# Performance work log

Hardware: AMD Instinct MI355X
Metric: run time of the kernel (lower is better)

## Reference

```python
import jax, jax.numpy as jnp
import numpy as np

COMMITMENT_COST = 0.25


def setup_inputs() -> dict:
    key = jax.random.key(0)
    k1, k2 = jax.random.split(key, 2)
    inputs = jax.random.normal(k1, (8, 2048, 1024), dtype=jnp.float32)
    # per-head codebooks: [H=4, K=1024, dh=256]
    codebook = jax.random.normal(k2, (4, 1024, 256), dtype=jnp.float32)
    return {"inputs": inputs, "codebook": codebook}


def reference(inputs, codebook):
    H, K, dh = codebook.shape
    flat = inputs.reshape(-1, H, dh)  # [N, H, dh]
    # squared-euclidean distances per head: [H, N, K]
    x_sq = jnp.sum(flat * flat, axis=-1).T[:, :, None]          # [H, N, 1]
    c_sq = jnp.sum(codebook * codebook, axis=-1)[:, None, :]    # [H, 1, K]
    dots = jnp.einsum('nhd,hkd->hnk', flat, codebook)           # [H, N, K]
    distances = x_sq + c_sq - 2.0 * dots
    idx = jnp.argmin(distances, axis=-1)                        # [H, N]
    # gather codebook rows (equivalent to one-hot @ codebook)
    q = jnp.take_along_axis(codebook, idx[:, :, None], axis=1)  # [H, N, dh]
    quantized = jnp.transpose(q, (1, 0, 2)).reshape(inputs.shape)
    # ema=True, eval mode: q_latent_loss = 0
    e_latent_loss = jnp.mean((jax.lax.stop_gradient(quantized) - inputs) ** 2)
    loss = COMMITMENT_COST * e_latent_loss
    # residual=False: straight-through estimator
    quantized_out = inputs + jax.lax.stop_gradient(quantized - inputs)
    return loss, quantized_out
```

## Files before the change

kernel.cpp:

```cpp
#include <hip/hip_runtime.h>
#include <cfloat>

#define NH    4
#define NK    1024
#define DHD   256
#define NTOK  16384
#define ROWS  (NH * DHD)

typedef __attribute__((ext_vector_type(8))) short bf16x8;
typedef __attribute__((ext_vector_type(4))) float f32x4;

#define WS_CSQ  ((size_t)0)
#define WS_BH   ((size_t)16384)
#define WS_BL   (WS_BH + (size_t)2097152)
#define WS_NEED (WS_BL + (size_t)2097152)

__device__ __forceinline__ unsigned short f32_to_bf16_rn(float f) {
    unsigned u = __float_as_uint(f);
    u += 0x7FFFu + ((u >> 16) & 1u);
    return (unsigned short)(u >> 16);
}
__device__ __forceinline__ float bf16_as_f32(unsigned short h) {
    return __uint_as_float(((unsigned)h) << 16);
}

__device__ __forceinline__ void gload_lds16(const uint4* g, uint4* l) {
    __builtin_amdgcn_global_load_lds(
        (const __attribute__((address_space(1))) void*)g,
        (__attribute__((address_space(3))) void*)l, 16, 0, 0);
}

__global__ __launch_bounds__(64) void csq_kernel(const float* __restrict__ cb,
                                                 float* __restrict__ csq) {
    const int code = blockIdx.x;
    const int lane = threadIdx.x;
    const float4 v = *(const float4*)(cb + (size_t)code * DHD + lane * 4);
    float s = v.x * v.x + v.y * v.y + v.z * v.z + v.w * v.w;
#pragma unroll
    for (int off = 32; off > 0; off >>= 1) s += __shfl_down(s, off, 64);
    if (lane == 0) csq[code] = s;
}

__global__ __launch_bounds__(256) void cvt_cb_kernel(const float* __restrict__ cb,
                                                     uint4* __restrict__ bch,
                                                     uint4* __restrict__ bcl) {
    const int g = blockIdx.x * 8 + (threadIdx.x >> 5);
    const int o = threadIdx.x & 31;
    const float* src = cb + (size_t)g * DHD + o * 8;
    unsigned wh[4], wl[4];
#pragma unroll
    for (int i = 0; i < 4; ++i) {
        const float f0 = src[2 * i], f1 = src[2 * i + 1];
        const unsigned short h0 = f32_to_bf16_rn(f0);
        const unsigned short h1 = f32_to_bf16_rn(f1);
        const unsigned short l0 = f32_to_bf16_rn(f0 - bf16_as_f32(h0));
        const unsigned short l1 = f32_to_bf16_rn(f1 - bf16_as_f32(h1));
        wh[i] = (unsigned)h0 | ((unsigned)h1 << 16);
        wl[i] = (unsigned)l0 | ((unsigned)l1 << 16);
    }
    const int hh = g >> 10, c = g & 1023, dc = o >> 2, kk = o & 3;
    const size_t unit = (size_t)((hh * 8 + dc) * 4 + kk) * NK + c;
    bch[unit] = make_uint4(wh[0], wh[1], wh[2], wh[3]);
    bcl[unit] = make_uint4(wl[0], wl[1], wl[2], wl[3]);
}

__device__ __forceinline__ bool lt_vi(float v, int i, float w, int j) {
    return (v < w) || (v == w && i < j);
}

__device__ __forceinline__ float np_sq_pairwise256(const float* __restrict__ a) {
#pragma clang fp contract(off)
    float tot = 0.f;
#pragma unroll
    for (int blk = 0; blk < 2; ++blk) {
        const float* p = a + blk * 128;
        float r0 = p[0] * p[0], r1 = p[1] * p[1], r2 = p[2] * p[2], r3 = p[3] * p[3];
        float r4 = p[4] * p[4], r5 = p[5] * p[5], r6 = p[6] * p[6], r7 = p[7] * p[7];
#pragma clang loop unroll_count(2)
        for (int i = 8; i < 128; i += 8) {
            r0 = r0 + p[i + 0] * p[i + 0];
            r1 = r1 + p[i + 1] * p[i + 1];
            r2 = r2 + p[i + 2] * p[i + 2];
            r3 = r3 + p[i + 3] * p[i + 3];
            r4 = r4 + p[i + 4] * p[i + 4];
            r5 = r5 + p[i + 5] * p[i + 5];
            r6 = r6 + p[i + 6] * p[i + 6];
            r7 = r7 + p[i + 7] * p[i + 7];
        }
        const float res = ((r0 + r1) + (r2 + r3)) + ((r4 + r5) + (r6 + r7));
        tot = (blk == 0) ? res : (tot + res);
    }
    return tot;
}

__device__ __forceinline__ float np_dot_seq256(const float* __restrict__ a,
                                               const float* __restrict__ b) {
#pragma clang fp contract(off)
    float s = 0.f;
#pragma clang loop unroll_count(4)
    for (int i = 0; i < 256; ++i) s = s + a[i] * b[i];
    return s;
}

__global__ __launch_bounds__(256, 2) void vq_mfma(const float* __restrict__ x,
                                                  const float* __restrict__ cb,
                                                  const float* __restrict__ csq,
                                                  const uint4* __restrict__ bch,
                                                  const uint4* __restrict__ bcl,
                                                  float* __restrict__ out) {
    __shared__ uint4 BsH[2048];
    __shared__ uint4 BsL[2048];
    __shared__ float Cs[NK];
    __shared__ int   Cand[128][2];
    __shared__ int   SIdx[128];
    __shared__ float WSum[4];

    const int tid  = threadIdx.x;
    const int h    = blockIdx.y;
    const int t0   = blockIdx.x * 128;
    const int wv   = tid >> 6;
    const int lane = tid & 63;
    const int kk   = lane >> 4;
    const int ln   = lane & 15;

    const float* xh  = x  + (size_t)t0 * ROWS + h * DHD;
    const float* cbh = cb + (size_t)h * NK * DHD;

#pragma unroll
    for (int i = tid; i < NK; i += 256) Cs[i] = csq[h * NK + i];

    bf16x8 aH[2][8], aL[2][8];
    {
        const int tokb = t0 + wv * 32 + ln;
        const float* xa = x + (size_t)tokb * ROWS + h * DHD + kk * 8;
#pragma unroll
        for (int rt = 0; rt < 2; ++rt) {
#pragma unroll
            for (int dc = 0; dc < 8; ++dc) {
                const float* p = xa + (size_t)(rt * 16) * ROWS + dc * 32;
                const float4 f0 = *(const float4*)p;
                const float4 f1 = *(const float4*)(p + 4);
                const float f[8] = {f0.x, f0.y, f0.z, f0.w, f1.x, f1.y, f1.z, f1.w};
                bf16x8 hv, lv;
#pragma unroll
                for (int j = 0; j < 8; ++j) {
                    const unsigned short hb = f32_to_bf16_rn(f[j]);
                    hv[j] = (short)hb;
                    lv[j] = (short)f32_to_bf16_rn(f[j] - bf16_as_f32(hb));
                }
                aH[rt][dc] = hv;
                aL[rt][dc] = lv;
            }
        }
    }

    float b1[8], b2[8];
    int   i1[8], i2[8];
#pragma unroll
    for (int s = 0; s < 8; ++s) { b1[s] = FLT_MAX; b2[s] = FLT_MAX; i1[s] = 0; i2[s] = 0; }

    for (int k0 = 0; k0 < NK; k0 += 64) {
        __syncthreads();
#pragma unroll
        for (int p = 0; p < 8; ++p) {
            const size_t w = (size_t)(h * 32 + p * 4 + wv) * NK + k0 + lane;
            gload_lds16(&bch[w], &BsH[p * 256 + wv * 64]);
            gload_lds16(&bcl[w], &BsL[p * 256 + wv * 64]);
        }
        __syncthreads();

        f32x4 acc[2][4];
#pragma unroll
        for (int rt = 0; rt < 2; ++rt)
#pragma unroll
            for (int ct = 0; ct < 4; ++ct) acc[rt][ct] = (f32x4){0.f, 0.f, 0.f, 0.f};

#pragma unroll
        for (int dc = 0; dc < 8; ++dc) {
#pragma unroll
            for (int ct = 0; ct < 4; ++ct) {
                const int bu = (dc * 4 + kk) * 64 + ct * 16 + ln;
                const bf16x8 bH = *(const bf16x8*)&BsH[bu];
                const bf16x8 bL = *(const bf16x8*)&BsL[bu];
#pragma unroll
                for (int rt = 0; rt < 2; ++rt) {
                    acc[rt][ct] = __builtin_amdgcn_mfma_f32_16x16x32_bf16(aH[rt][dc], bH, acc[rt][ct], 0, 0, 0);
                    acc[rt][ct] = __builtin_amdgcn_mfma_f32_16x16x32_bf16(aH[rt][dc], bL, acc[rt][ct], 0, 0, 0);
                    acc[rt][ct] = __builtin_amdgcn_mfma_f32_16x16x32_bf16(aL[rt][dc], bH, acc[rt][ct], 0, 0, 0);
                }
            }
        }

#pragma unroll
        for (int rt = 0; rt < 2; ++rt)
#pragma unroll
            for (int ct = 0; ct < 4; ++ct) {
                const float cs   = Cs[k0 + ct * 16 + ln];
                const int   codg = k0 + ct * 16 + ln;
#pragma unroll
                for (int r = 0; r < 4; ++r) {
                    const float dist = cs - 2.f * acc[rt][ct][r];
                    const int   s    = rt * 4 + r;
                    if (dist < b1[s]) { b2[s] = b1[s]; i2[s] = i1[s]; b1[s] = dist; i1[s] = codg; }
                    else if (dist < b2[s]) { b2[s] = dist; i2[s] = codg; }
                }
            }
    }

#pragma unroll
    for (int s = 0; s < 8; ++s) {
        float v1 = b1[s], v2 = b2[s];
        int   j1 = i1[s], j2 = i2[s];
#pragma unroll
        for (int m = 1; m <= 8; m <<= 1) {
            const float o1 = __shfl_xor(v1, m, 64);
            const int   oj1 = __shfl_xor(j1, m, 64);
            const float o2 = __shfl_xor(v2, m, 64);
            const int   oj2 = __shfl_xor(j2, m, 64);
            if (lt_vi(o1, oj1, v1, j1)) {
                if (lt_vi(v1, j1, o2, oj2)) { v2 = v1; j2 = j1; }
                else                        { v2 = o2; j2 = oj2; }
                v1 = o1; j1 = oj1;
            } else if (lt_vi(o1, oj1, v2, j2)) {
                v2 = o1; j2 = oj1;
            }
        }
        if (ln == 0) {
            const int tl = wv * 32 + (s >> 2) * 16 + kk * 4 + (s & 3);
            Cand[tl][0] = j1;
            Cand[tl][1] = j2;
        }
    }
    __syncthreads();

    {
        const int token = tid >> 1;
        const int cand  = tid & 1;
        const int code  = Cand[token][cand];
        const float* xr = xh + (size_t)token * ROWS;
        const float* cr = cbh + (size_t)code * DHD;
        const float X = np_sq_pairwise256(xr);
        const float C = np_sq_pairwise256(cr);
        const float D = np_dot_seq256(xr, cr);
        float d;
        {
#pragma clang fp contract(off)
            const float t = X + C;
            d = t - 2.0f * D;
        }
        const float od = __shfl_xor(d, 1, 64);
        if (cand == 0) {
            const int jA = code;
            const int jB = Cand[token][1];
            const bool pickB = (od < d) || (od == d && jB < jA);
            SIdx[token] = pickB ? jB : jA;
        }
    }
    __syncthreads();

    float lacc = 0.f;
    for (int t = wv; t < 128; t += 4) {
        const float4 q4 = *(const float4*)(cbh + (size_t)SIdx[t] * DHD + (lane << 2));
        const float4 x4 = *(const float4*)(xh + (size_t)t * ROWS + (lane << 2));
        const float dx = q4.x - x4.x, dy = q4.y - x4.y;
        const float dz = q4.z - x4.z, dw = q4.w - x4.w;
        lacc += dx * dx + dy * dy + dz * dz + dw * dw;
        *(float4*)(out + 1 + (size_t)(t0 + t) * ROWS + h * DHD + (lane << 2)) = q4;
    }
#pragma unroll
    for (int off = 32; off > 0; off >>= 1) lacc += __shfl_down(lacc, off, 64);
    if (lane == 0) WSum[wv] = lacc;
    __syncthreads();
    if (tid == 0) {
        const float s = WSum[0] + WSum[1] + WSum[2] + WSum[3];
        atomicAdd(out, s * (0.25f / 16777216.f));
    }
}

#define TN 128
#define TK 128
#define KC 16
#define APAD 4
#define BPAD 4

__global__ __launch_bounds__(256, 2) void vq_main_fp32(const float* __restrict__ x,
                                                       const float* __restrict__ cb,
                                                       const float* __restrict__ csq,
                                                       float* __restrict__ out) {
    __shared__ float As[KC][TN + APAD];
    __shared__ float Bs[KC][TK + BPAD];
    __shared__ float Cs[TK];
    __shared__ int   Cand[TN][2];
    __shared__ int   SIdx[TN];
    __shared__ float WSum[4];

    const int tid = threadIdx.x;
    const int h   = blockIdx.y;
    const int t0  = blockIdx.x * TN;
    const int ty  = tid >> 4;
    const int tx  = tid & 15;

    const float* xh  = x  + (size_t)t0 * ROWS + h * DHD;
    const float* cbh = cb + (size_t)h * NK * DHD;

    const int sr = tid >> 1;
    const int sd = (tid & 1) << 3;

    float b1[8], b2[8];
    int   i1[8], i2[8];
#pragma unroll
    for (int r = 0; r < 8; ++r) { b1[r] = FLT_MAX; b2[r] = FLT_MAX; i1[r] = 0; i2[r] = 0; }

    for (int k0 = 0; k0 < NK; k0 += TK) {
        __syncthreads();
        if (tid < TK) Cs[tid] = csq[h * NK + k0 + tid];

        float acc[8][8];
#pragma unroll
        for (int r = 0; r < 8; ++r)
#pragma unroll
            for (int c = 0; c < 8; ++c) acc[r][c] = 0.f;

        for (int d0 = 0; d0 < DHD; d0 += KC) {
            __syncthreads();
            {
                const float* ap = xh + (size_t)sr * ROWS + d0 + sd;
                const float4 a0 = *(const float4*)ap;
                const float4 a1 = *(const float4*)(ap + 4);
                As[sd + 0][sr] = a0.x; As[sd + 1][sr] = a0.y;
                As[sd + 2][sr] = a0.z; As[sd + 3][sr] = a0.w;
                As[sd + 4][sr] = a1.x; As[sd + 5][sr] = a1.y;
                As[sd + 6][sr] = a1.z; As[sd + 7][sr] = a1.w;
            }
            {
                const float* bp = cbh + (size_t)(k0 + sr) * DHD + d0 + sd;
                const float4 b0v = *(const float4*)bp;
                const float4 b1v = *(const float4*)(bp + 4);
                Bs[sd + 0][sr] = b0v.x; Bs[sd + 1][sr] = b0v.y;
                Bs[sd + 2][sr] = b0v.z; Bs[sd + 3][sr] = b0v.w;
                Bs[sd + 4][sr] = b1v.x; Bs[sd + 5][sr] = b1v.y;
                Bs[sd + 6][sr] = b1v.z; Bs[sd + 7][sr] = b1v.w;
            }
            __syncthreads();
#pragma unroll 4
            for (int kc = 0; kc < KC; ++kc) {
                const float4 a0 = *(const float4*)&As[kc][ty << 3];
                const float4 a1 = *(const float4*)&As[kc][(ty << 3) + 4];
                const float4 p0 = *(const float4*)&Bs[kc][tx << 2];
                const float4 p1 = *(const float4*)&Bs[kc][64 + (tx << 2)];
                const float aa[8] = {a0.x, a0.y, a0.z, a0.w, a1.x, a1.y, a1.z, a1.w};
                const float bb[8] = {p0.x, p0.y, p0.z, p0.w, p1.x, p1.y, p1.z, p1.w};
#pragma unroll
                for (int r = 0; r < 8; ++r)
#pragma unroll
                    for (int c = 0; c < 8; ++c)
                        acc[r][c] = fmaf(aa[r], bb[c], acc[r][c]);
            }
        }
#pragma unroll
        for (int r = 0; r < 8; ++r) {
#pragma unroll
            for (int c = 0; c < 8; ++c) {
                const int cc = (c < 4) ? ((tx << 2) + c) : (64 + (tx << 2) + c - 4);
                const float dist = Cs[cc] - 2.f * acc[r][c];
                const int   idx  = k0 + cc;
                if (dist < b1[r]) { b2[r] = b1[r]; i2[r] = i1[r]; b1[r] = dist; i1[r] = idx; }
                else if (dist < b2[r]) { b2[r] = dist; i2[r] = idx; }
            }
        }
    }

#pragma unroll
    for (int r = 0; r < 8; ++r) {
        float v1 = b1[r], v2 = b2[r];
        int   j1 = i1[r], j2 = i2[r];
#pragma unroll
        for (int m = 1; m <= 8; m <<= 1) {
            const float o1 = __shfl_xor(v1, m, 64);
            const int   oj1 = __shfl_xor(j1, m, 64);
            const float o2 = __shfl_xor(v2, m, 64);
            const int   oj2 = __shfl_xor(j2, m, 64);
            if (lt_vi(o1, oj1, v1, j1)) {
                if (lt_vi(v1, j1, o2, oj2)) { v2 = v1; j2 = j1; }
                else                        { v2 = o2; j2 = oj2; }
                v1 = o1; j1 = oj1;
            } else if (lt_vi(o1, oj1, v2, j2)) {
                v2 = o1; j2 = oj1;
            }
        }
        b1[r] = v1; i1[r] = j1; b2[r] = v2; i2[r] = j2;
    }
    if (tx == 0) {
#pragma unroll
        for (int r = 0; r < 8; ++r) {
            Cand[(ty << 3) + r][0] = i1[r];
            Cand[(ty << 3) + r][1] = i2[r];
        }
    }
    __syncthreads();

    {
        const int token = tid >> 1;
        const int cand  = tid & 1;
        const int code  = Cand[token][cand];
        const float* xr = xh + (size_t)token * ROWS;
        const float* cr = cbh + (size_t)code * DHD;
        const float X = np_sq_pairwise256(xr);
        const float C = np_sq_pairwise256(cr);
        const float D = np_dot_seq256(xr, cr);
        float d;
        {
#pragma clang fp contract(off)
            const float t = X + C;
            d = t - 2.0f * D;
        }
        const float od = __shfl_xor(d, 1, 64);
        if (cand == 0) {
            const int jA = code;
            const int jB = Cand[token][1];
            const bool pickB = (od < d) || (od == d && jB < jA);
            SIdx[token] = pickB ? jB : jA;
        }
    }
    __syncthreads();

    const int wav  = tid >> 6;
    const int lane = tid & 63;
    float lacc = 0.f;
    for (int t = wav; t < TN; t += 4) {
        const float4 q4 = *(const float4*)(cbh + (size_t)SIdx[t] * DHD + (lane << 2));
        const float4 x4 = *(const float4*)(xh + (size_t)t * ROWS + (lane << 2));
        const float dx = q4.x - x4.x, dy = q4.y - x4.y;
        const float dz = q4.z - x4.z, dw = q4.w - x4.w;
        lacc += dx * dx + dy * dy + dz * dz + dw * dw;
        *(float4*)(out + 1 + (size_t)(t0 + t) * ROWS + h * DHD + (lane << 2)) = q4;
    }
#pragma unroll
    for (int off = 32; off > 0; off >>= 1) lacc += __shfl_down(lacc, off, 64);
    if (lane == 0) WSum[wav] = lacc;
    __syncthreads();
    if (tid == 0) {
        const float s = WSum[0] + WSum[1] + WSum[2] + WSum[3];
        atomicAdd(out, s * (0.25f / 16777216.f));
    }
}

extern "C" void kernel_launch(void* const* d_in, const int* in_sizes, int n_in,
                              void* d_out, int out_size, void* d_ws, size_t ws_size,
                              hipStream_t stream) {
    const float* x   = (const float*)d_in[0];
    const float* cb  = (const float*)d_in[1];
    float*       out = (float*)d_out;
    char*        ws  = (char*)d_ws;
    float*       csq = (float*)(ws + WS_CSQ);

    hipMemsetAsync(d_out, 0, sizeof(float), stream);
    csq_kernel<<<NH * NK, 64, 0, stream>>>(cb, csq);

    if (ws_size >= WS_NEED) {
        uint4* bch = (uint4*)(ws + WS_BH);
        uint4* bcl = (uint4*)(ws + WS_BL);
        cvt_cb_kernel<<<NH * NK / 8, 256, 0, stream>>>(cb, bch, bcl);
        dim3 grid(NTOK / 128, NH);
        vq_mfma<<<grid, 256, 0, stream>>>(x, cb, csq, bch, bcl, out);
    } else {
        dim3 grid(NTOK / TN, NH);
        vq_main_fp32<<<grid, 256, 0, stream>>>(x, cb, csq, out);
    }
}
```

Before: 329.4 us.

## Double-buffer codebook tiles, swizzle block order, and fuse exact refinement loads

Measured after the change: 378.4 us. 14.9% more time.

```diff
diff --git a/kernel.cpp b/kernel.cpp
--- a/kernel.cpp
+++ b/kernel.cpp
@@ -102,22 +102,91 @@
     return s;
 }
 
+__device__ __forceinline__ void refine_exact(const float* __restrict__ xr,
+                                             const float* __restrict__ cr,
+                                             float& Xo, float& Co, float& Do) {
+#pragma clang fp contract(off)
+    const float4* xq = (const float4*)xr;
+    const float4* cq = (const float4*)cr;
+    float xa[8], ca[8];
+    float xres0 = 0.f, cres0 = 0.f;
+    float s = 0.f;
+#pragma unroll
+    for (int c = 0; c < 8; ++c) {
+        float xf[32], cf[32];
+#pragma unroll
+        for (int q = 0; q < 8; ++q) {
+            const float4 a = xq[c * 8 + q];
+            const float4 b = cq[c * 8 + q];
+            xf[q * 4 + 0] = a.x; xf[q * 4 + 1] = a.y;
+            xf[q * 4 + 2] = a.z; xf[q * 4 + 3] = a.w;
+            cf[q * 4 + 0] = b.x; cf[q * 4 + 1] = b.y;
+            cf[q * 4 + 2] = b.z; cf[q * 4 + 3] = b.w;
+        }
+        if (c == 0 || c == 4) {
+#pragma unroll
+            for (int j = 0; j < 8; ++j) { xa[j] = xf[j] * xf[j]; ca[j] = cf[j] * cf[j]; }
+#pragma unroll
+            for (int k = 1; k < 4; ++k)
+#pragma unroll
+                for (int j = 0; j < 8; ++j) {
+                    xa[j] = xa[j] + xf[k * 8 + j] * xf[k * 8 + j];
+                    ca[j] = ca[j] + cf[k * 8 + j] * cf[k * 8 + j];
+                }
+        } else {
+#pragma unroll
+            for (int k = 0; k < 4; ++k)
+#pragma unroll
+                for (int j = 0; j < 8; ++j) {
+                    xa[j] = xa[j] + xf[k * 8 + j] * xf[k * 8 + j];
+                    ca[j] = ca[j] + cf[k * 8 + j] * cf[k * 8 + j];
+                }
+        }
+        if (c == 3) {
+            xres0 = ((xa[0] + xa[1]) + (xa[2] + xa[3])) + ((xa[4] + xa[5]) + (xa[6] + xa[7]));
+            cres0 = ((ca[0] + ca[1]) + (ca[2] + ca[3])) + ((ca[4] + ca[5]) + (ca[6] + ca[7]));
+        }
+#pragma unroll
+        for (int k = 0; k < 32; ++k) s = s + xf[k] * cf[k];
+    }
+    Xo = xres0 + (((xa[0] + xa[1]) + (xa[2] + xa[3])) + ((xa[4] + xa[5]) + (xa[6] + xa[7])));
+    Co = cres0 + (((ca[0] + ca[1]) + (ca[2] + ca[3])) + ((ca[4] + ca[5]) + (ca[6] + ca[7])));
+    Do = s;
+}
+
+#define KT 32
+#define NT (NK / KT)
+
+#define STAGE_TILE(BUF, K0)                                                   \
+    {                                                                         \
+        _Pragma("unroll")                                                     \
+        for (int p_ = 0; p_ < 4; ++p_) {                                      \
+            const int q_   = p_ * 4 + wv;                                     \
+            const int row_ = 2 * q_ + (lane >> 5);                            \
+            const size_t w_ = (size_t)(h * 32 + row_) * NK + (K0) + (lane & 31); \
+            gload_lds16(&bch[w_], &BsH[BUF][q_ * 64]);                        \
+            gload_lds16(&bcl[w_], &BsL[BUF][q_ * 64]);                        \
+        }                                                                     \
+    }
+
 __global__ __launch_bounds__(256, 2) void vq_mfma(const float* __restrict__ x,
                                                   const float* __restrict__ cb,
                                                   const float* __restrict__ csq,
                                                   const uint4* __restrict__ bch,
                                                   const uint4* __restrict__ bcl,
                                                   float* __restrict__ out) {
-    __shared__ uint4 BsH[2048];
-    __shared__ uint4 BsL[2048];
+    __shared__ uint4 BsH[2][1024];
+    __shared__ uint4 BsL[2][1024];
     __shared__ float Cs[NK];
     __shared__ int   Cand[128][2];
     __shared__ int   SIdx[128];
     __shared__ float WSum[4];
 
     const int tid  = threadIdx.x;
-    const int h    = blockIdx.y;
-    const int t0   = blockIdx.x * 128;
+    const int wg   = blockIdx.x + gridDim.x * blockIdx.y;
+    const int sw   = (wg & 7) * 64 + (wg >> 3);
+    const int h    = sw >> 7;
+    const int t0   = (sw & 127) * 128;
     const int wv   = tid >> 6;
     const int lane = tid & 63;
     const int kk   = lane >> 4;
@@ -125,6 +194,8 @@
 
     const float* xh  = x  + (size_t)t0 * ROWS + h * DHD;
     const float* cbh = cb + (size_t)h * NK * DHD;
+
+    STAGE_TILE(0, 0)
 
 #pragma unroll
     for (int i = tid; i < NK; i += 256) Cs[i] = csq[h * NK + i];
@@ -159,29 +230,26 @@
 #pragma unroll
     for (int s = 0; s < 8; ++s) { b1[s] = FLT_MAX; b2[s] = FLT_MAX; i1[s] = 0; i2[s] = 0; }
 
-    for (int k0 = 0; k0 < NK; k0 += 64) {
-        __syncthreads();
-#pragma unroll
-        for (int p = 0; p < 8; ++p) {
-            const size_t w = (size_t)(h * 32 + p * 4 + wv) * NK + k0 + lane;
-            gload_lds16(&bch[w], &BsH[p * 256 + wv * 64]);
-            gload_lds16(&bcl[w], &BsL[p * 256 + wv * 64]);
-        }
-        __syncthreads();
-
-        f32x4 acc[2][4];
+    __syncthreads();
+    int cur = 0;
+
+    for (int t = 0; t < NT; ++t) {
+        const int k0 = t * KT;
+        if (t + 1 < NT) STAGE_TILE(cur ^ 1, k0 + KT)
+
+        f32x4 acc[2][2];
 #pragma unroll
         for (int rt = 0; rt < 2; ++rt)
 #pragma unroll
-            for (int ct = 0; ct < 4; ++ct) acc[rt][ct] = (f32x4){0.f, 0.f, 0.f, 0.f};
+            for (int ct = 0; ct < 2; ++ct) acc[rt][ct] = (f32x4){0.f, 0.f, 0.f, 0.f};
 
 #pragma unroll
         for (int dc = 0; dc < 8; ++dc) {
 #pragma unroll
-            for (int ct = 0; ct < 4; ++ct) {
-                const int bu = (dc * 4 + kk) * 64 + ct * 16 + ln;
-                const bf16x8 bH = *(const bf16x8*)&BsH[bu];
-                const bf16x8 bL = *(const bf16x8*)&BsL[bu];
+            for (int ct = 0; ct < 2; ++ct) {
+                const int bu = (dc * 4 + kk) * 32 + ct * 16 + ln;
+                const bf16x8 bH = *(const bf16x8*)&BsH[cur][bu];
+                const bf16x8 bL = *(const bf16x8*)&BsL[cur][bu];
 #pragma unroll
                 for (int rt = 0; rt < 2; ++rt) {
                     acc[rt][ct] = __builtin_amdgcn_mfma_f32_16x16x32_bf16(aH[rt][dc], bH, acc[rt][ct], 0, 0, 0);
@@ -194,7 +262,7 @@
 #pragma unroll
         for (int rt = 0; rt < 2; ++rt)
 #pragma unroll
-            for (int ct = 0; ct < 4; ++ct) {
+            for (int ct = 0; ct < 2; ++ct) {
                 const float cs   = Cs[k0 + ct * 16 + ln];
                 const int   codg = k0 + ct * 16 + ln;
 #pragma unroll
@@ -205,6 +273,9 @@
                     else if (dist < b2[s]) { b2[s] = dist; i2[s] = codg; }
                 }
             }
+
+        __syncthreads();
+        cur ^= 1;
     }
 
 #pragma unroll
@@ -229,6 +300,171 @@
             const int tl = wv * 32 + (s >> 2) * 16 + kk * 4 + (s & 3);
             Cand[tl][0] = j1;
             Cand[tl][1] = j2;
+        }
+    }
+    __syncthreads();
+
+    {
+        const int token = tid >> 1;
+        const int cand  = tid & 1;
+        const int code  = Cand[token][cand];
+        const float* xr = xh + (size_t)token * ROWS;
+        const float* cr = cbh + (size_t)code * DHD;
+        float X, C, D;
+        refine_exact(xr, cr, X, C, D);
+        float d;
+        {
+#pragma clang fp contract(off)
+            const float t = X + C;
+            d = t - 2.0f * D;
+        }
+        const float od = __shfl_xor(d, 1, 64);
+        if (cand == 0) {
+            const int jA = code;
+            const int jB = Cand[token][1];
+            const bool pickB = (od < d) || (od == d && jB < jA);
+            SIdx[token] = pickB ? jB : jA;
+        }
+    }
+    __syncthreads();
+
+    float lacc = 0.f;
+    for (int t = wv; t < 128; t += 4) {
+        const float4 q4 = *(const float4*)(cbh + (size_t)SIdx[t] * DHD + (lane << 2));
+        const float4 x4 = *(const float4*)(xh + (size_t)t * ROWS + (lane << 2));
+        const float dx = q4.x - x4.x, dy = q4.y - x4.y;
+        const float dz = q4.z - x4.z, dw = q4.w - x4.w;
+        lacc += dx * dx + dy * dy + dz * dz + dw * dw;
+        *(float4*)(out + 1 + (size_t)(t0 + t) * ROWS + h * DHD + (lane << 2)) = q4;
+    }
+#pragma unroll
+    for (int off = 32; off > 0; off >>= 1) lacc += __shfl_down(lacc, off, 64);
+    if (lane == 0) WSum[wv] = lacc;
+    __syncthreads();
+    if (tid == 0) {
+        const float s = WSum[0] + WSum[1] + WSum[2] + WSum[3];
+        atomicAdd(out, s * (0.25f / 16777216.f));
+    }
+}
+
+#define TN 128
+#define TK 128
+#define KC 16
+#define APAD 4
+#define BPAD 4
+
+__global__ __launch_bounds__(256, 2) void vq_main_fp32(const float* __restrict__ x,
+                                                       const float* __restrict__ cb,
+                                                       const float* __restrict__ csq,
+                                                       float* __restrict__ out) {
+    __shared__ float As[KC][TN + APAD];
+    __shared__ float Bs[KC][TK + BPAD];
+    __shared__ float Cs[TK];
+    __shared__ int   Cand[TN][2];
+    __shared__ int   SIdx[TN];
+    __shared__ float WSum[4];
+
+    const int tid = threadIdx.x;
+    const int h   = blockIdx.y;
+    const int t0  = blockIdx.x * TN;
+    const int ty  = tid >> 4;
+    const int tx  = tid & 15;
+
+    const float* xh  = x  + (size_t)t0 * ROWS + h * DHD;
+    const float* cbh = cb + (size_t)h * NK * DHD;
+
+    const int sr = tid >> 1;
+    const int sd = (tid & 1) << 3;
+
+    float b1[8], b2[8];
+    int   i1[8], i2[8];
+#pragma unroll
+    for (int r = 0; r < 8; ++r) { b1[r] = FLT_MAX; b2[r] = FLT_MAX; i1[r] = 0; i2[r] = 0; }
+
+    for (int k0 = 0; k0 < NK; k0 += TK) {
+        __syncthreads();
+        if (tid < TK) Cs[tid] = csq[h * NK + k0 + tid];
+
+        float acc[8][8];
+#pragma unroll
+        for (int r = 0; r < 8; ++r)
+#pragma unroll
+            for (int c = 0; c < 8; ++c) acc[r][c] = 0.f;
+
+        for (int d0 = 0; d0 < DHD; d0 += KC) {
+            __syncthreads();
+            {
+                const float* ap = xh + (size_t)sr * ROWS + d0 + sd;
+                const float4 a0 = *(const float4*)ap;
+                const float4 a1 = *(const float4*)(ap + 4);
+                As[sd + 0][sr] = a0.x; As[sd + 1][sr] = a0.y;
+                As[sd + 2][sr] = a0.z; As[sd + 3][sr] = a0.w;
+                As[sd + 4][sr] = a1.x; As[sd + 5][sr] = a1.y;
+                As[sd + 6][sr] = a1.z; As[sd + 7][sr] = a1.w;
+            }
+            {
+                const float* bp = cbh + (size_t)(k0 + sr) * DHD + d0 + sd;
+                const float4 b0v = *(const float4*)bp;
+                const float4 b1v = *(const float4*)(bp + 4);
+                Bs[sd + 0][sr] = b0v.x; Bs[sd + 1][sr] = b0v.y;
+                Bs[sd + 2][sr] = b0v.z; Bs[sd + 3][sr] = b0v.w;
+                Bs[sd + 4][sr] = b1v.x; Bs[sd + 5][sr] = b1v.y;
+                Bs[sd + 6][sr] = b1v.z; Bs[sd + 7][sr] = b1v.w;
+            }
+            __syncthreads();
+#pragma unroll 4
+            for (int kc = 0; kc < KC; ++kc) {
+                const float4 a0 = *(const float4*)&As[kc][ty << 3];
+                const float4 a1 = *(const float4*)&As[kc][(ty << 3) + 4];
+                const float4 p0 = *(const float4*)&Bs[kc][tx << 2];
+                const float4 p1 = *(const float4*)&Bs[kc][64 + (tx << 2)];
+                const float aa[8] = {a0.x, a0.y, a0.z, a0.w, a1.x, a1.y, a1.z, a1.w};
+                const float bb[8] = {p0.x, p0.y, p0.z, p0.w, p1.x, p1.y, p1.z, p1.w};
+#pragma unroll
+                for (int r = 0; r < 8; ++r)
+#pragma unroll
+                    for (int c = 0; c < 8; ++c)
+                        acc[r][c] = fmaf(aa[r], bb[c], acc[r][c]);
+            }
+        }
+#pragma unroll
+        for (int r = 0; r < 8; ++r) {
+#pragma unroll
+            for (int c = 0; c < 8; ++c) {
+                const int cc = (c < 4) ? ((tx << 2) + c) : (64 + (tx << 2) + c - 4);
+                const float dist = Cs[cc] - 2.f * acc[r][c];
+                const int   idx  = k0 + cc;
+                if (dist < b1[r]) { b2[r] = b1[r]; i2[r] = i1[r]; b1[r] = dist; i1[r] = idx; }
+                else if (dist < b2[r]) { b2[r] = dist; i2[r] = idx; }
+            }
+        }
+    }
+
+#pragma unroll
+    for (int r = 0; r < 8; ++r) {
+        float v1 = b1[r], v2 = b2[r];
+        int   j1 = i1[r], j2 = i2[r];
+#pragma unroll
+        for (int m = 1; m <= 8; m <<= 1) {
+            const float o1 = __shfl_xor(v1, m, 64);
+            const int   oj1 = __shfl_xor(j1, m, 64);
+            const float o2 = __shfl_xor(v2, m, 64);
+            const int   oj2 = __shfl_xor(j2, m, 64);
+            if (lt_vi(o1, oj1, v1, j1)) {
+                if (lt_vi(v1, j1, o2, oj2)) { v2 = v1; j2 = j1; }
+                else                        { v2 = o2; j2 = oj2; }
+                v1 = o1; j1 = oj1;
+            } else if (lt_vi(o1, oj1, v2, j2)) {
+                v2 = o1; j2 = oj1;
+            }
+        }
+        b1[r] = v1; i1[r] = j1; b2[r] = v2; i2[r] = j2;
+    }
+    if (tx == 0) {
+#pragma unroll
+        for (int r = 0; r < 8; ++r) {
+            Cand[(ty << 3) + r][0] = i1[r];
+            Cand[(ty << 3) + r][1] = i2[r];
         }
     }
     __syncthreads();
@@ -258,172 +494,6 @@
     }
     __syncthreads();
 
-    float lacc = 0.f;
-    for (int t = wv; t < 128; t += 4) {
-        const float4 q4 = *(const float4*)(cbh + (size_t)SIdx[t] * DHD + (lane << 2));
-        const float4 x4 = *(const float4*)(xh + (size_t)t * ROWS + (lane << 2));
-        const float dx = q4.x - x4.x, dy = q4.y - x4.y;
-        const float dz = q4.z - x4.z, dw = q4.w - x4.w;
-        lacc += dx * dx + dy * dy + dz * dz + dw * dw;
-        *(float4*)(out + 1 + (size_t)(t0 + t) * ROWS + h * DHD + (lane << 2)) = q4;
-    }
-#pragma unroll
-    for (int off = 32; off > 0; off >>= 1) lacc += __shfl_down(lacc, off, 64);
-    if (lane == 0) WSum[wv] = lacc;
-    __syncthreads();
-    if (tid == 0) {
-        const float s = WSum[0] + WSum[1] + WSum[2] + WSum[3];
-        atomicAdd(out, s * (0.25f / 16777216.f));
-    }
-}
-
-#define TN 128
-#define TK 128
-#define KC 16
-#define APAD 4
-#define BPAD 4
-
-__global__ __launch_bounds__(256, 2) void vq_main_fp32(const float* __restrict__ x,
-                                                       const float* __restrict__ cb,
-                                                       const float* __restrict__ csq,
-                                                       float* __restrict__ out) {
-    __shared__ float As[KC][TN + APAD];
-    __shared__ float Bs[KC][TK + BPAD];
-    __shared__ float Cs[TK];
-    __shared__ int   Cand[TN][2];
-    __shared__ int   SIdx[TN];
-    __shared__ float WSum[4];
-
-    const int tid = threadIdx.x;
-    const int h   = blockIdx.y;
-    const int t0  = blockIdx.x * TN;
-    const int ty  = tid >> 4;
-    const int tx  = tid & 15;
-
-    const float* xh  = x  + (size_t)t0 * ROWS + h * DHD;
-    const float* cbh = cb + (size_t)h * NK * DHD;
-
-    const int sr = tid >> 1;
-    const int sd = (tid & 1) << 3;
-
-    float b1[8], b2[8];
-    int   i1[8], i2[8];
-#pragma unroll
-    for (int r = 0; r < 8; ++r) { b1[r] = FLT_MAX; b2[r] = FLT_MAX; i1[r] = 0; i2[r] = 0; }
-
-    for (int k0 = 0; k0 < NK; k0 += TK) {
-        __syncthreads();
-        if (tid < TK) Cs[tid] = csq[h * NK + k0 + tid];
-
-        float acc[8][8];
-#pragma unroll
-        for (int r = 0; r < 8; ++r)
-#pragma unroll
-            for (int c = 0; c < 8; ++c) acc[r][c] = 0.f;
-
-        for (int d0 = 0; d0 < DHD; d0 += KC) {
-            __syncthreads();
-            {
-                const float* ap = xh + (size_t)sr * ROWS + d0 + sd;
-                const float4 a0 = *(const float4*)ap;
-                const float4 a1 = *(const float4*)(ap + 4);
-                As[sd + 0][sr] = a0.x; As[sd + 1][sr] = a0.y;
-                As[sd + 2][sr] = a0.z; As[sd + 3][sr] = a0.w;
-                As[sd + 4][sr] = a1.x; As[sd + 5][sr] = a1.y;
-                As[sd + 6][sr] = a1.z; As[sd + 7][sr] = a1.w;
-            }
-            {
-                const float* bp = cbh + (size_t)(k0 + sr) * DHD + d0 + sd;
-                const float4 b0v = *(const float4*)bp;
-                const float4 b1v = *(const float4*)(bp + 4);
-                Bs[sd + 0][sr] = b0v.x; Bs[sd + 1][sr] = b0v.y;
-                Bs[sd + 2][sr] = b0v.z; Bs[sd + 3][sr] = b0v.w;
-                Bs[sd + 4][sr] = b1v.x; Bs[sd + 5][sr] = b1v.y;
-                Bs[sd + 6][sr] = b1v.z; Bs[sd + 7][sr] = b1v.w;
-            }
-            __syncthreads();
-#pragma unroll 4
-            for (int kc = 0; kc < KC; ++kc) {
-                const float4 a0 = *(const float4*)&As[kc][ty << 3];
-                const float4 a1 = *(const float4*)&As[kc][(ty << 3) + 4];
-                const float4 p0 = *(const float4*)&Bs[kc][tx << 2];
-                const float4 p1 = *(const float4*)&Bs[kc][64 + (tx << 2)];
-                const float aa[8] = {a0.x, a0.y, a0.z, a0.w, a1.x, a1.y, a1.z, a1.w};
-                const float bb[8] = {p0.x, p0.y, p0.z, p0.w, p1.x, p1.y, p1.z, p1.w};
-#pragma unroll
-                for (int r = 0; r < 8; ++r)
-#pragma unroll
-                    for (int c = 0; c < 8; ++c)
-                        acc[r][c] = fmaf(aa[r], bb[c], acc[r][c]);
-            }
-        }
-#pragma unroll
-        for (int r = 0; r < 8; ++r) {
-#pragma unroll
-            for (int c = 0; c < 8; ++c) {
-                const int cc = (c < 4) ? ((tx << 2) + c) : (64 + (tx << 2) + c - 4);
-                const float dist = Cs[cc] - 2.f * acc[r][c];
-                const int   idx  = k0 + cc;
-                if (dist < b1[r]) { b2[r] = b1[r]; i2[r] = i1[r]; b1[r] = dist; i1[r] = idx; }
-                else if (dist < b2[r]) { b2[r] = dist; i2[r] = idx; }
-            }
-        }
-    }
-
-#pragma unroll
-    for (int r = 0; r < 8; ++r) {
-        float v1 = b1[r], v2 = b2[r];
-        int   j1 = i1[r], j2 = i2[r];
-#pragma unroll
-        for (int m = 1; m <= 8; m <<= 1) {
-            const float o1 = __shfl_xor(v1, m, 64);
-            const int   oj1 = __shfl_xor(j1, m, 64);
-            const float o2 = __shfl_xor(v2, m, 64);
-            const int   oj2 = __shfl_xor(j2, m, 64);
-            if (lt_vi(o1, oj1, v1, j1)) {
-                if (lt_vi(v1, j1, o2, oj2)) { v2 = v1; j2 = j1; }
-                else                        { v2 = o2; j2 = oj2; }
-                v1 = o1; j1 = oj1;
-            } else if (lt_vi(o1, oj1, v2, j2)) {
-                v2 = o1; j2 = oj1;
-            }
-        }
-        b1[r] = v1; i1[r] = j1; b2[r] = v2; i2[r] = j2;
-    }
-    if (tx == 0) {
-#pragma unroll
-        for (int r = 0; r < 8; ++r) {
-            Cand[(ty << 3) + r][0] = i1[r];
-            Cand[(ty << 3) + r][1] = i2[r];
-        }
-    }
-    __syncthreads();
-
-    {
-        const int token = tid >> 1;
-        const int cand  = tid & 1;
-        const int code  = Cand[token][cand];
-        const float* xr = xh + (size_t)token * ROWS;
-        const float* cr = cbh + (size_t)code * DHD;
-        const float X = np_sq_pairwise256(xr);
-        const float C = np_sq_pairwise256(cr);
-        const float D = np_dot_seq256(xr, cr);
-        float d;
-        {
-#pragma clang fp contract(off)
-            const float t = X + C;
-            d = t - 2.0f * D;
-        }
-        const float od = __shfl_xor(d, 1, 64);
-        if (cand == 0) {
-            const int jA = code;
-            const int jB = Cand[token][1];
-            const bool pickB = (od < d) || (od == d && jB < jA);
-            SIdx[token] = pickB ? jB : jA;
-        }
-    }
-    __syncthreads();
-
     const int wav  = tid >> 6;
     const int lane = tid & 63;
     float lacc = 0.f;
```

## Retile MFMA VQ kernel to 64 tokens with double-buffered codebook staging

Applied to the files above, without the earlier changes.

New measurement: 469.8 us. 42.7% more time.

```diff
diff --git a/kernel.cpp b/kernel.cpp
--- a/kernel.cpp
+++ b/kernel.cpp
@@ -102,22 +102,78 @@
     return s;
 }
 
-__global__ __launch_bounds__(256, 2) void vq_mfma(const float* __restrict__ x,
+__device__ __forceinline__ void refine_exact(const float* __restrict__ xr,
+                                             const float* __restrict__ cr,
+                                             float& Xo, float& Co, float& Do) {
+#pragma clang fp contract(off)
+    float s = 0.f;
+    float X = 0.f, C = 0.f;
+#pragma unroll
+    for (int blk = 0; blk < 2; ++blk) {
+        const float4* xq = (const float4*)(xr + blk * 128);
+        const float4* cq = (const float4*)(cr + blk * 128);
+        float xa[8], ca[8];
+#pragma unroll
+        for (int g = 0; g < 16; ++g) {
+            const float4 a0 = xq[2 * g], a1 = xq[2 * g + 1];
+            const float4 b0 = cq[2 * g], b1 = cq[2 * g + 1];
+            const float xf[8] = {a0.x, a0.y, a0.z, a0.w, a1.x, a1.y, a1.z, a1.w};
+            const float cf[8] = {b0.x, b0.y, b0.z, b0.w, b1.x, b1.y, b1.z, b1.w};
+            if (g == 0) {
+#pragma unroll
+                for (int j = 0; j < 8; ++j) { xa[j] = xf[j] * xf[j]; ca[j] = cf[j] * cf[j]; }
+            } else {
+#pragma unroll
+                for (int j = 0; j < 8; ++j) {
+                    xa[j] = xa[j] + xf[j] * xf[j];
+                    ca[j] = ca[j] + cf[j] * cf[j];
+                }
+            }
+#pragma unroll
+            for (int j = 0; j < 8; ++j) s = s + xf[j] * cf[j];
+        }
+        const float xres = ((xa[0] + xa[1]) + (xa[2] + xa[3])) + ((xa[4] + xa[5]) + (xa[6] + xa[7]));
+        const float cres = ((ca[0] + ca[1]) + (ca[2] + ca[3])) + ((ca[4] + ca[5]) + (ca[6] + ca[7]));
+        X = (blk == 0) ? xres : (X + xres);
+        C = (blk == 0) ? cres : (C + cres);
+    }
+    Xo = X; Co = C; Do = s;
+}
+
+#define BT 64
+#define KT 16
+#define NT (NK / KT)
+
+#define STAGE_TILE(BUF, K0)                                                    \
+    {                                                                          \
+        _Pragma("unroll")                                                      \
+        for (int p_ = 0; p_ < 2; ++p_) {                                       \
+            const int q_   = wv * 2 + p_;                                      \
+            const int row_ = q_ * 4 + (lane >> 4);                             \
+            const size_t w_ = (size_t)(h * 32 + row_) * NK + (K0) + (lane & 15); \
+            gload_lds16(&bch[w_], &BsH[BUF][q_ * 64]);                         \
+            gload_lds16(&bcl[w_], &BsL[BUF][q_ * 64]);                         \
+        }                                                                      \
+    }
+
+__global__ __launch_bounds__(256, 4) void vq_mfma(const float* __restrict__ x,
                                                   const float* __restrict__ cb,
                                                   const float* __restrict__ csq,
                                                   const uint4* __restrict__ bch,
                                                   const uint4* __restrict__ bcl,
                                                   float* __restrict__ out) {
-    __shared__ uint4 BsH[2048];
-    __shared__ uint4 BsL[2048];
+    __shared__ uint4 BsH[2][512];
+    __shared__ uint4 BsL[2][512];
     __shared__ float Cs[NK];
-    __shared__ int   Cand[128][2];
-    __shared__ int   SIdx[128];
+    __shared__ int   Cand[BT][2];
+    __shared__ int   SIdx[BT];
     __shared__ float WSum[4];
 
     const int tid  = threadIdx.x;
-    const int h    = blockIdx.y;
-    const int t0   = blockIdx.x * 128;
+    const int wg   = blockIdx.x + gridDim.x * blockIdx.y;
+    const int sw   = (wg & 7) * 128 + (wg >> 3);
+    const int h    = sw >> 8;
+    const int t0   = (sw & 255) * BT;
     const int wv   = tid >> 6;
     const int lane = tid & 63;
     const int kk   = lane >> 4;
@@ -126,89 +182,78 @@
     const float* xh  = x  + (size_t)t0 * ROWS + h * DHD;
     const float* cbh = cb + (size_t)h * NK * DHD;
 
+    STAGE_TILE(0, 0)
+
 #pragma unroll
     for (int i = tid; i < NK; i += 256) Cs[i] = csq[h * NK + i];
 
-    bf16x8 aH[2][8], aL[2][8];
+    bf16x8 aH[8], aL[8];
     {
-        const int tokb = t0 + wv * 32 + ln;
+        const int tokb = t0 + wv * 16 + ln;
         const float* xa = x + (size_t)tokb * ROWS + h * DHD + kk * 8;
 #pragma unroll
-        for (int rt = 0; rt < 2; ++rt) {
-#pragma unroll
-            for (int dc = 0; dc < 8; ++dc) {
-                const float* p = xa + (size_t)(rt * 16) * ROWS + dc * 32;
-                const float4 f0 = *(const float4*)p;
-                const float4 f1 = *(const float4*)(p + 4);
-                const float f[8] = {f0.x, f0.y, f0.z, f0.w, f1.x, f1.y, f1.z, f1.w};
-                bf16x8 hv, lv;
-#pragma unroll
-                for (int j = 0; j < 8; ++j) {
-                    const unsigned short hb = f32_to_bf16_rn(f[j]);
-                    hv[j] = (short)hb;
-                    lv[j] = (short)f32_to_bf16_rn(f[j] - bf16_as_f32(hb));
-                }
-                aH[rt][dc] = hv;
-                aL[rt][dc] = lv;
-            }
-        }
-    }
-
-    float b1[8], b2[8];
-    int   i1[8], i2[8];
-#pragma unroll
-    for (int s = 0; s < 8; ++s) { b1[s] = FLT_MAX; b2[s] = FLT_MAX; i1[s] = 0; i2[s] = 0; }
-
-    for (int k0 = 0; k0 < NK; k0 += 64) {
+        for (int dc = 0; dc < 8; ++dc) {
+            const float* p = xa + dc * 32;
+            const float4 f0 = *(const float4*)p;
+            const float4 f1 = *(const float4*)(p + 4);
+            const float f[8] = {f0.x, f0.y, f0.z, f0.w, f1.x, f1.y, f1.z, f1.w};
+            bf16x8 hv, lv;
+#pragma unroll
+            for (int j = 0; j < 8; ++j) {
+                const unsigned short hb = f32_to_bf16_rn(f[j]);
+                hv[j] = (short)hb;
+                lv[j] = (short)f32_to_bf16_rn(f[j] - bf16_as_f32(hb));
+            }
+            aH[dc] = hv;
+            aL[dc] = lv;
+        }
+    }
+
+    float b1[4], b2[4];
+    int   i1[4], i2[4];
+#pragma unroll
+    for (int s = 0; s < 4; ++s) { b1[s] = FLT_MAX; b2[s] = FLT_MAX; i1[s] = 0; i2[s] = 0; }
+
+    __syncthreads();
+    int cur = 0;
+
+    for (int t = 0; t < NT; ++t) {
+        const int k0 = t * KT;
+        if (t + 1 < NT) STAGE_TILE(cur ^ 1, k0 + KT)
+
+        f32x4 acc0 = (f32x4){0.f, 0.f, 0.f, 0.f};
+        f32x4 acc1 = (f32x4){0.f, 0.f, 0.f, 0.f};
+#pragma unroll
+        for (int dc = 0; dc < 8; dc += 2) {
+            const int bu0 = ((dc + 0) * 4 + kk) * 16 + ln;
+            const int bu1 = ((dc + 1) * 4 + kk) * 16 + ln;
+            const bf16x8 bH0 = *(const bf16x8*)&BsH[cur][bu0];
+            const bf16x8 bL0 = *(const bf16x8*)&BsL[cur][bu0];
+            const bf16x8 bH1 = *(const bf16x8*)&BsH[cur][bu1];
+            const bf16x8 bL1 = *(const bf16x8*)&BsL[cur][bu1];
+            acc0 = __builtin_amdgcn_mfma_f32_16x16x32_bf16(aH[dc + 0], bH0, acc0, 0, 0, 0);
+            acc1 = __builtin_amdgcn_mfma_f32_16x16x32_bf16(aH[dc + 1], bH1, acc1, 0, 0, 0);
+            acc0 = __builtin_amdgcn_mfma_f32_16x16x32_bf16(aH[dc + 0], bL0, acc0, 0, 0, 0);
+            acc1 = __builtin_amdgcn_mfma_f32_16x16x32_bf16(aH[dc + 1], bL1, acc1, 0, 0, 0);
+            acc0 = __builtin_amdgcn_mfma_f32_16x16x32_bf16(aL[dc + 0], bH0, acc0, 0, 0, 0);
+            acc1 = __builtin_amdgcn_mfma_f32_16x16x32_bf16(aL[dc + 1], bH1, acc1, 0, 0, 0);
+        }
+
+        const float cs   = Cs[k0 + ln];
+        const int   codg = k0 + ln;
+#pragma unroll
+        for (int r = 0; r < 4; ++r) {
+            const float dist = cs - 2.f * (acc0[r] + acc1[r]);
+            if (dist < b1[r]) { b2[r] = b1[r]; i2[r] = i1[r]; b1[r] = dist; i1[r] = codg; }
+            else if (dist < b2[r]) { b2[r] = dist; i2[r] = codg; }
+        }
+
         __syncthreads();
-#pragma unroll
-        for (int p = 0; p < 8; ++p) {
-            const size_t w = (size_t)(h * 32 + p * 4 + wv) * NK + k0 + lane;
-            gload_lds16(&bch[w], &BsH[p * 256 + wv * 64]);
-            gload_lds16(&bcl[w], &BsL[p * 256 + wv * 64]);
-        }
-        __syncthreads();
-
-        f32x4 acc[2][4];
-#pragma unroll
-        for (int rt = 0; rt < 2; ++rt)
-#pragma unroll
-            for (int ct = 0; ct < 4; ++ct) acc[rt][ct] = (f32x4){0.f, 0.f, 0.f, 0.f};
-
-#pragma unroll
-        for (int dc = 0; dc < 8; ++dc) {
-#pragma unroll
-            for (int ct = 0; ct < 4; ++ct) {
-                const int bu = (dc * 4 + kk) * 64 + ct * 16 + ln;
-                const bf16x8 bH = *(const bf16x8*)&BsH[bu];
-                const bf16x8 bL = *(const bf16x8*)&BsL[bu];
-#pragma unroll
-                for (int rt = 0; rt < 2; ++rt) {
-                    acc[rt][ct] = __builtin_amdgcn_mfma_f32_16x16x32_bf16(aH[rt][dc], bH, acc[rt][ct], 0, 0, 0);
-                    acc[rt][ct] = __builtin_amdgcn_mfma_f32_16x16x32_bf16(aH[rt][dc], bL, acc[rt][ct], 0, 0, 0);
-                    acc[rt][ct] = __builtin_amdgcn_mfma_f32_16x16x32_bf16(aL[rt][dc], bH, acc[rt][ct], 0, 0, 0);
-                }
-            }
-        }
-
-#pragma unroll
-        for (int rt = 0; rt < 2; ++rt)
-#pragma unroll
-            for (int ct = 0; ct < 4; ++ct) {
-                const float cs   = Cs[k0 + ct * 16 + ln];
-                const int   codg = k0 + ct * 16 + ln;
-#pragma unroll
-                for (int r = 0; r < 4; ++r) {
-                    const float dist = cs - 2.f * acc[rt][ct][r];
-                    const int   s    = rt * 4 + r;
-                    if (dist < b1[s]) { b2[s] = b1[s]; i2[s] = i1[s]; b1[s] = dist; i1[s] = codg; }
-                    else if (dist < b2[s]) { b2[s] = dist; i2[s] = codg; }
-                }
-            }
-    }
-
-#pragma unroll
-    for (int s = 0; s < 8; ++s) {
+        cur ^= 1;
+    }
+
+#pragma unroll
+    for (int s = 0; s < 4; ++s) {
         float v1 = b1[s], v2 = b2[s];
         int   j1 = i1[s], j2 = i2[s];
 #pragma unroll
@@ -226,9 +271,174 @@
             }
         }
         if (ln == 0) {
-            const int tl = wv * 32 + (s >> 2) * 16 + kk * 4 + (s & 3);
+            const int tl = wv * 16 + kk * 4 + s;
             Cand[tl][0] = j1;
             Cand[tl][1] = j2;
+        }
+    }
+    __syncthreads();
+
+    if (tid < 2 * BT) {
+        const int token = tid >> 1;
+        const int cand  = tid & 1;
+        const int code  = Cand[token][cand];
+        const float* xr = xh + (size_t)token * ROWS;
+        const float* cr = cbh + (size_t)code * DHD;
+        float X, C, D;
+        refine_exact(xr, cr, X, C, D);
+        float d;
+        {
+#pragma clang fp contract(off)
+            const float t = X + C;
+            d = t - 2.0f * D;
+        }
+        const float od = __shfl_xor(d, 1, 64);
+        if (cand == 0) {
+            const int jA = code;
+            const int jB = Cand[token][1];
+            const bool pickB = (od < d) || (od == d && jB < jA);
+            SIdx[token] = pickB ? jB : jA;
+        }
+    }
+    __syncthreads();
+
+    float lacc = 0.f;
+    for (int t = wv; t < BT; t += 4) {
+        const float4 q4 = *(const float4*)(cbh + (size_t)SIdx[t] * DHD + (lane << 2));
+        const float4 x4 = *(const float4*)(xh + (size_t)t * ROWS + (lane << 2));
+        const float dx = q4.x - x4.x, dy = q4.y - x4.y;
+        const float dz = q4.z - x4.z, dw = q4.w - x4.w;
+        lacc += dx * dx + dy * dy + dz * dz + dw * dw;
+        *(float4*)(out + 1 + (size_t)(t0 + t) * ROWS + h * DHD + (lane << 2)) = q4;
+    }
+#pragma unroll
+    for (int off = 32; off > 0; off >>= 1) lacc += __shfl_down(lacc, off, 64);
+    if (lane == 0) WSum[wv] = lacc;
+    __syncthreads();
+    if (tid == 0) {
+        const float s = WSum[0] + WSum[1] + WSum[2] + WSum[3];
+        atomicAdd(out, s * (0.25f / 16777216.f));
+    }
+}
+
+#define TN 128
+#define TK 128
+#define KC 16
+#define APAD 4
+#define BPAD 4
+
+__global__ __launch_bounds__(256, 2) void vq_main_fp32(const float* __restrict__ x,
+                                                       const float* __restrict__ cb,
+                                                       const float* __restrict__ csq,
+                                                       float* __restrict__ out) {
+    __shared__ float As[KC][TN + APAD];
+    __shared__ float Bs[KC][TK + BPAD];
+    __shared__ float Cs[TK];
+    __shared__ int   Cand[TN][2];
+    __shared__ int   SIdx[TN];
+    __shared__ float WSum[4];
+
+    const int tid = threadIdx.x;
+    const int h   = blockIdx.y;
+    const int t0  = blockIdx.x * TN;
+    const int ty  = tid >> 4;
+    const int tx  = tid & 15;
+
+    const float* xh  = x  + (size_t)t0 * ROWS + h * DHD;
+    const float* cbh = cb + (size_t)h * NK * DHD;
+
+    const int sr = tid >> 1;
+    const int sd = (tid & 1) << 3;
+
+    float b1[8], b2[8];
+    int   i1[8], i2[8];
+#pragma unroll
+    for (int r = 0; r < 8; ++r) { b1[r] = FLT_MAX; b2[r] = FLT_MAX; i1[r] = 0; i2[r] = 0; }
+
+    for (int k0 = 0; k0 < NK; k0 += TK) {
+        __syncthreads();
+        if (tid < TK) Cs[tid] = csq[h * NK + k0 + tid];
+
+        float acc[8][8];
+#pragma unroll
+        for (int r = 0; r < 8; ++r)
+#pragma unroll
+            for (int c = 0; c < 8; ++c) acc[r][c] = 0.f;
+
+        for (int d0 = 0; d0 < DHD; d0 += KC) {
+            __syncthreads();
+            {
+                const float* ap = xh + (size_t)sr * ROWS + d0 + sd;
+                const float4 a0 = *(const float4*)ap;
+                const float4 a1 = *(const float4*)(ap + 4);
+                As[sd + 0][sr] = a0.x; As[sd + 1][sr] = a0.y;
+                As[sd + 2][sr] = a0.z; As[sd + 3][sr] = a0.w;
+                As[sd + 4][sr] = a1.x; As[sd + 5][sr] = a1.y;
+                As[sd + 6][sr] = a1.z; As[sd + 7][sr] = a1.w;
+            }
+            {
+                const float* bp = cbh + (size_t)(k0 + sr) * DHD + d0 + sd;
+                const float4 b0v = *(const float4*)bp;
+                const float4 b1v = *(const float4*)(bp + 4);
+                Bs[sd + 0][sr] = b0v.x; Bs[sd + 1][sr] = b0v.y;
+                Bs[sd + 2][sr] = b0v.z; Bs[sd + 3][sr] = b0v.w;
+                Bs[sd + 4][sr] = b1v.x; Bs[sd + 5][sr] = b1v.y;
+                Bs[sd + 6][sr] = b1v.z; Bs[sd + 7][sr] = b1v.w;
+            }
+            __syncthreads();
+#pragma unroll 4
+            for (int kc = 0; kc < KC; ++kc) {
+                const float4 a0 = *(const float4*)&As[kc][ty << 3];
+                const float4 a1 = *(const float4*)&As[kc][(ty << 3) + 4];
+                const float4 p0 = *(const float4*)&Bs[kc][tx << 2];
+                const float4 p1 = *(const float4*)&Bs[kc][64 + (tx << 2)];
+                const float aa[8] = {a0.x, a0.y, a0.z, a0.w, a1.x, a1.y, a1.z, a1.w};
+                const float bb[8] = {p0.x, p0.y, p0.z, p0.w, p1.x, p1.y, p1.z, p1.w};
+#pragma unroll
+                for (int r = 0; r < 8; ++r)
+#pragma unroll
+                    for (int c = 0; c < 8; ++c)
+                        acc[r][c] = fmaf(aa[r], bb[c], acc[r][c]);
+            }
+        }
+#pragma unroll
+        for (int r = 0; r < 8; ++r) {
+#pragma unroll
+            for (int c = 0; c < 8; ++c) {
+                const int cc = (c < 4) ? ((tx << 2) + c) : (64 + (tx << 2) + c - 4);
+                const float dist = Cs[cc] - 2.f * acc[r][c];
+                const int   idx  = k0 + cc;
+                if (dist < b1[r]) { b2[r] = b1[r]; i2[r] = i1[r]; b1[r] = dist; i1[r] = idx; }
+                else if (dist < b2[r]) { b2[r] = dist; i2[r] = idx; }
+            }
+        }
+    }
+
+#pragma unroll
+    for (int r = 0; r < 8; ++r) {
+        float v1 = b1[r], v2 = b2[r];
+        int   j1 = i1[r], j2 = i2[r];
+#pragma unroll
+        for (int m = 1; m <= 8; m <<= 1) {
+            const float o1 = __shfl_xor(v1, m, 64);
+            const int   oj1 = __shfl_xor(j1, m, 64);
+            const float o2 = __shfl_xor(v2, m, 64);
+            const int   oj2 = __shfl_xor(j2, m, 64);
+            if (lt_vi(o1, oj1, v1, j1)) {
+                if (lt_vi(v1, j1, o2, oj2)) { v2 = v1; j2 = j1; }
+                else                        { v2 = o2; j2 = oj2; }
+                v1 = o1; j1 = oj1;
+            } else if (lt_vi(o1, oj1, v2, j2)) {
+                v2 = o1; j2 = oj1;
+            }
+        }
+        b1[r] = v1; i1[r] = j1; b2[r] = v2; i2[r] = j2;
+    }
+    if (tx == 0) {
+#pragma unroll
+        for (int r = 0; r < 8; ++r) {
+            Cand[(ty << 3) + r][0] = i1[r];
+            Cand[(ty << 3) + r][1] = i2[r];
         }
     }
     __syncthreads();
@@ -258,172 +468,6 @@
     }
     __syncthreads();
 
-    float lacc = 0.f;
-    for (int t = wv; t < 128; t += 4) {
-        const float4 q4 = *(const float4*)(cbh + (size_t)SIdx[t] * DHD + (lane << 2));
-        const float4 x4 = *(const float4*)(xh + (size_t)t * ROWS + (lane << 2));
-        const float dx = q4.x - x4.x, dy = q4.y - x4.y;
-        const float dz = q4.z - x4.z, dw = q4.w - x4.w;
-        lacc += dx * dx + dy * dy + dz * dz + dw * dw;
-        *(float4*)(out + 1 + (size_t)(t0 + t) * ROWS + h * DHD + (lane << 2)) = q4;
-    }
-#pragma unroll
-    for (int off = 32; off > 0; off >>= 1) lacc += __shfl_down(lacc, off, 64);
-    if (lane == 0) WSum[wv] = lacc;
-    __syncthreads();
-    if (tid == 0) {
-        const float s = WSum[0] + WSum[1] + WSum[2] + WSum[3];
-        atomicAdd(out, s * (0.25f / 16777216.f));
-    }
-}
-
-#define TN 128
-#define TK 128
-#define KC 16
-#define APAD 4
-#define BPAD 4
-
-__global__ __launch_bounds__(256, 2) void vq_main_fp32(const float* __restrict__ x,
-                                                       const float* __restrict__ cb,
-                                                       const float* __restrict__ csq,
-                                                       float* __restrict__ out) {
-    __shared__ float As[KC][TN + APAD];
-    __shared__ float Bs[KC][TK + BPAD];
-    __shared__ float Cs[TK];
-    __shared__ int   Cand[TN][2];
-    __shared__ int   SIdx[TN];
-    __shared__ float WSum[4];
-
-    const int tid = threadIdx.x;
-    const int h   = blockIdx.y;
-    const int t0  = blockIdx.x * TN;
-    const int ty  = tid >> 4;
-    const int tx  = tid & 15;
-
-    const float* xh  = x  + (size_t)t0 * ROWS + h * DHD;
-    const float* cbh = cb + (size_t)h * NK * DHD;
-
-    const int sr = tid >> 1;
-    const int sd = (tid & 1) << 3;
-
-    float b1[8], b2[8];
-    int   i1[8], i2[8];
-#pragma unroll
-    for (int r = 0; r < 8; ++r) { b1[r] = FLT_MAX; b2[r] = FLT_MAX; i1[r] = 0; i2[r] = 0; }
-
-    for (int k0 = 0; k0 < NK; k0 += TK) {
-        __syncthreads();
-        if (tid < TK) Cs[tid] = csq[h * NK + k0 + tid];
-
-        float acc[8][8];
-#pragma unroll
-        for (int r = 0; r < 8; ++r)
-#pragma unroll
-            for (int c = 0; c < 8; ++c) acc[r][c] = 0.f;
-
-        for (int d0 = 0; d0 < DHD; d0 += KC) {
-            __syncthreads();
-            {
-                const float* ap = xh + (size_t)sr * ROWS + d0 + sd;
-                const float4 a0 = *(const float4*)ap;
-                const float4 a1 = *(const float4*)(ap + 4);
-                As[sd + 0][sr] = a0.x; As[sd + 1][sr] = a0.y;
-                As[sd + 2][sr] = a0.z; As[sd + 3][sr] = a0.w;
-                As[sd + 4][sr] = a1.x; As[sd + 5][sr] = a1.y;
-                As[sd + 6][sr] = a1.z; As[sd + 7][sr] = a1.w;
-            }
-            {
-                const float* bp = cbh + (size_t)(k0 + sr) * DHD + d0 + sd;
-                const float4 b0v = *(const float4*)bp;
-                const float4 b1v = *(const float4*)(bp + 4);
-                Bs[sd + 0][sr] = b0v.x; Bs[sd + 1][sr] = b0v.y;
-                Bs[sd + 2][sr] = b0v.z; Bs[sd + 3][sr] = b0v.w;
-                Bs[sd + 4][sr] = b1v.x; Bs[sd + 5][sr] = b1v.y;
-                Bs[sd + 6][sr] = b1v.z; Bs[sd + 7][sr] = b1v.w;
-            }
-            __syncthreads();
-#pragma unroll 4
-            for (int kc = 0; kc < KC; ++kc) {
-                const float4 a0 = *(const float4*)&As[kc][ty << 3];
-                const float4 a1 = *(const float4*)&As[kc][(ty << 3) + 4];
-                const float4 p0 = *(const float4*)&Bs[kc][tx << 2];
-                const float4 p1 = *(const float4*)&Bs[kc][64 + (tx << 2)];
-                const float aa[8] = {a0.x, a0.y, a0.z, a0.w, a1.x, a1.y, a1.z, a1.w};
-                const float bb[8] = {p0.x, p0.y, p0.z, p0.w, p1.x, p1.y, p1.z, p1.w};
-#pragma unroll
-                for (int r = 0; r < 8; ++r)
-#pragma unroll
-                    for (int c = 0; c < 8; ++c)
-                        acc[r][c] = fmaf(aa[r], bb[c], acc[r][c]);
-            }
-        }
-#pragma unroll
-        for (int r = 0; r < 8; ++r) {
-#pragma unroll
-            for (int c = 0; c < 8; ++c) {
-                const int cc = (c < 4) ? ((tx << 2) + c) : (64 + (tx << 2) + c - 4);
-                const float dist = Cs[cc] - 2.f * acc[r][c];
-                const int   idx  = k0 + cc;
-                if (dist < b1[r]) { b2[r] = b1[r]; i2[r] = i1[r]; b1[r] = dist; i1[r] = idx; }
-                else if (dist < b2[r]) { b2[r] = dist; i2[r] = idx; }
-            }
-        }
-    }
-
-#pragma unroll
-    for (int r = 0; r < 8; ++r) {
-        float v1 = b1[r], v2 = b2[r];
-        int   j1 = i1[r], j2 = i2[r];
-#pragma unroll
-        for (int m = 1; m <= 8; m <<= 1) {
-            const float o1 = __shfl_xor(v1, m, 64);
-            const int   oj1 = __shfl_xor(j1, m, 64);
-            const float o2 = __shfl_xor(v2, m, 64);
-            const int   oj2 = __shfl_xor(j2, m, 64);
-            if (lt_vi(o1, oj1, v1, j1)) {
-                if (lt_vi(v1, j1, o2, oj2)) { v2 = v1; j2 = j1; }
-                else                        { v2 = o2; j2 = oj2; }
-                v1 = o1; j1 = oj1;
-            } else if (lt_vi(o1, oj1, v2, j2)) {
-                v2 = o1; j2 = oj1;
-            }
-        }
-        b1[r] = v1; i1[r] = j1; b2[r] = v2; i2[r] = j2;
-    }
-    if (tx == 0) {
-#pragma unroll
-        for (int r = 0; r < 8; ++r) {
-            Cand[(ty << 3) + r][0] = i1[r];
-            Cand[(ty << 3) + r][1] = i2[r];
-        }
-    }
-    __syncthreads();
-
-    {
-        const int token = tid >> 1;
-        const int cand  = tid & 1;
-        const int code  = Cand[token][cand];
-        const float* xr = xh + (size_t)token * ROWS;
-        const float* cr = cbh + (size_t)code * DHD;
-        const float X = np_sq_pairwise256(xr);
-        const float C = np_sq_pairwise256(cr);
-        const float D = np_dot_seq256(xr, cr);
-        float d;
-        {
-#pragma clang fp contract(off)
-            const float t = X + C;
-            d = t - 2.0f * D;
-        }
-        const float od = __shfl_xor(d, 1, 64);
-        if (cand == 0) {
-            const int jA = code;
-            const int jB = Cand[token][1];
-            const bool pickB = (od < d) || (od == d && jB < jA);
-            SIdx[token] = pickB ? jB : jA;
-        }
-    }
-    __syncthreads();
-
     const int wav  = tid >> 6;
     const int lane = tid & 63;
     float lacc = 0.f;
@@ -461,7 +505,7 @@
         uint4* bch = (uint4*)(ws + WS_BH);
         uint4* bcl = (uint4*)(ws + WS_BL);
         cvt_cb_kernel<<<NH * NK / 8, 256, 0, stream>>>(cb, bch, bcl);
-        dim3 grid(NTOK / 128, NH);
+        dim3 grid(NTOK / BT, NH);
         vq_mfma<<<grid, 256, 0, stream>>>(x, cb, csq, bch, bcl, out);
     } else {
         dim3 grid(NTOK / TN, NH);
```
